# Optimization experiments

Hardware: AMD Instinct MI355X
Metric: run time of the kernel (lower is better)

## Reference

```python
import jax, jax.numpy as jnp
import numpy as np

BS = 8192
NUM_CLASSES = 400
D = 768


def _bilin_from_14(m14, Y, X, eH, eW):
    # Value of bilinear-resize(m14 -> (eH,eW)) at integer pixel (Y,X), computed on the fly.
    # torch F.interpolate(align_corners=False): src = (dst+0.5)*in/out - 0.5, clamped at 0.
    # m14: (bs,14,14); Y,X: (bs,14) float integer-valued coords; eH,eW: (bs,) float.
    sy = jnp.maximum((Y + 0.5) * 14.0 / eH[:, None] - 0.5, 0.0)
    sx = jnp.maximum((X + 0.5) * 14.0 / eW[:, None] - 0.5, 0.0)
    r0f = jnp.floor(sy); c0f = jnp.floor(sx)
    r0 = r0f.astype(jnp.int32); r1 = jnp.minimum(r0 + 1, 13)
    c0 = c0f.astype(jnp.int32); c1 = jnp.minimum(c0 + 1, 13)
    fy = sy - r0f; fx = sx - c0f
    b = jnp.arange(m14.shape[0])[:, None, None]
    g00 = m14[b, r0[:, :, None], c0[:, None, :]]
    g01 = m14[b, r0[:, :, None], c1[:, None, :]]
    g10 = m14[b, r1[:, :, None], c0[:, None, :]]
    g11 = m14[b, r1[:, :, None], c1[:, None, :]]
    wy = fy[:, :, None]; wx = fx[:, None, :]
    return g00 * (1 - wy) * (1 - wx) + g01 * (1 - wy) * wx + g10 * wy * (1 - wx) + g11 * wy * wx


def _get_mask(attn, o_pos, e_pos):
    # Fused, fully-batched equivalent of the per-sample python loop:
    #   resize 14x14 -> (eH,eW) bilinear; crop (top,left,oH,oW); resize -> 14x14 bilinear.
    # The final resize only reads the intermediate grid at 4 integer points per output
    # pixel, so we evaluate those points lazily via _bilin_from_14 (exact, no Emax grid).
    bs = attn.shape[0]
    m14 = attn.reshape(bs, 14, 14)
    eH = e_pos[:, 2].astype(jnp.float32); eW = e_pos[:, 3].astype(jnp.float32)
    top = (o_pos[:, 0] - e_pos[:, 0]).astype(jnp.float32)
    left = (o_pos[:, 1] - e_pos[:, 1]).astype(jnp.float32)
    oH = o_pos[:, 2].astype(jnp.float32); oW = o_pos[:, 3].astype(jnp.float32)
    i = jnp.arange(14, dtype=jnp.float32)[None, :]
    ty = jnp.maximum((i + 0.5) * oH[:, None] / 14.0 - 0.5, 0.0)  # (bs,14) coords in crop
    tx = jnp.maximum((i + 0.5) * oW[:, None] / 14.0 - 0.5, 0.0)
    y0 = jnp.floor(ty); y1 = jnp.minimum(y0 + 1.0, oH[:, None] - 1.0); wy = ty - y0
    x0 = jnp.floor(tx); x1 = jnp.minimum(x0 + 1.0, oW[:, None] - 1.0); wx = tx - x0
    Y0 = top[:, None] + y0; Y1 = top[:, None] + y1  # absolute rows in (eH,eW) grid
    X0 = left[:, None] + x0; X1 = left[:, None] + x1
    v00 = _bilin_from_14(m14, Y0, X0, eH, eW)
    v01 = _bilin_from_14(m14, Y0, X1, eH, eW)
    v10 = _bilin_from_14(m14, Y1, X0, eH, eW)
    v11 = _bilin_from_14(m14, Y1, X1, eH, eW)
    wyc = wy[:, :, None]; wxc = wx[:, None, :]
    out = v00 * (1 - wyc) * (1 - wxc) + v01 * (1 - wyc) * wxc + v10 * wyc * (1 - wxc) + v11 * wyc * wxc
    return out.reshape(bs, 196)


def _get_att_mask(attention, ratio=0.5):
    bs = attention.shape[0]
    a14 = attention.reshape(bs, 14, 14)
    # bilinear 14->7 with align_corners=False samples at frac 0.5 == 2x2 average pool
    a7 = a14.reshape(bs, 7, 2, 7, 2).mean(axis=(2, 4))
    flat = a7.reshape(bs, 49)
    n_keep = int(49 * ratio) + 1  # argsort desc, take top N+1 = 25
    _, idx = jax.lax.top_k(flat, n_keep)
    masks = jnp.ones((bs, 49), dtype=bool)
    masks = masks.at[jnp.arange(bs)[:, None], idx].set(False)
    m7 = masks.reshape(bs, 7, 7)
    full = jnp.repeat(jnp.repeat(m7, 2, axis=1), 2, axis=2)
    return full.reshape(bs, 196)


def setup_inputs() -> dict:
    key = jax.random.key(0)
    k1, k2, k3 = jax.random.split(key, 3)
    attn = jax.random.uniform(k1, (BS, 196), dtype=jnp.float32)
    rng = np.random.default_rng(0)
    IMG = 224
    eH = rng.integers(112, IMG + 1, BS); eW = rng.integers(112, IMG + 1, BS)
    eT = rng.integers(0, IMG - eH + 1); eL = rng.integers(0, IMG - eW + 1)
    def box():
        h = rng.integers(56, eH + 1); w = rng.integers(56, eW + 1)
        t = eT + rng.integers(0, eH - h + 1); l = eL + rng.integers(0, eW - w + 1)
        return np.stack([t, l, h, w], axis=1)
    e = np.stack([eT, eL, eH, eW], axis=1)
    pos = np.stack([box(), box(), e], axis=1).astype(np.int32)  # (BS,3,4)
    image_embed = jax.random.normal(k2, (2 * BS, D), dtype=jnp.float32)
    W = jax.random.normal(k3, (NUM_CLASSES, D), dtype=jnp.float32) * 0.02
    b = jnp.zeros((NUM_CLASSES,), dtype=jnp.float32)
    return {"attn": attn, "pos": jnp.asarray(pos), "image_embed": image_embed, "W": W, "b": b}


def reference(attn, pos, image_embed, W, b):
    cm1 = _get_mask(attn, pos[:, 0], pos[:, 2])
    mask1 = _get_att_mask(cm1)
    cm2 = _get_mask(attn, pos[:, 1], pos[:, 2])
    mask2 = _get_att_mask(cm2)
    mask = jnp.concatenate([mask1, mask2], axis=0)  # (2*bs,196) bool, fed to masked encoder
    logits = image_embed @ W.T + b
    return logits, mask
```

## Files before the change

### kernel.cpp

```cpp
#include <hip/hip_runtime.h>
#include <hip/hip_bf16.h>
#include <stdint.h>
#include <type_traits>

#define BSAMP 8192
#define NCLS 400
#define DIM 768
#define LOGITS_SIZE (16384LL * 400LL)
#define GEMM_BLOCKS 256
#define MASK_BLOCKS 4096
#define W_ELEMS (NCLS * DIM)

typedef __attribute__((ext_vector_type(8))) short short8;
typedef __attribute__((ext_vector_type(4))) float floatx4;

__device__ inline unsigned int packbf(float a, float b) {
    unsigned int ua = __float_as_uint(a) + 0x8000u;
    unsigned int ub = __float_as_uint(b) + 0x8000u;
    return __builtin_amdgcn_perm(ub, ua, 0x07060302u);
}

__device__ inline short8 cvt8(float4 lo, float4 hi) {
    union { unsigned int u[4]; short8 s; } r;
    r.u[0] = packbf(lo.x, lo.y);
    r.u[1] = packbf(lo.z, lo.w);
    r.u[2] = packbf(hi.x, hi.y);
    r.u[3] = packbf(hi.z, hi.w);
    return r.s;
}

__device__ inline void gload16(const void* g, void* l) {
    __builtin_amdgcn_global_load_lds((const __attribute__((address_space(1))) void*)g,
                                     (__attribute__((address_space(3))) void*)l, 16, 0, 0);
}

__global__ void cvtW_kernel(const float* __restrict__ W, unsigned short* __restrict__ ws) {
    int i = (blockIdx.x * 256 + threadIdx.x) * 4;
    if (i < W_ELEMS) {
        float4 f = *(const float4*)(W + i);
        uint2 r;
        r.x = packbf(f.x, f.y);
        r.y = packbf(f.z, f.w);
        *(uint2*)(ws + i) = r;
    }
}

__device__ inline float tap4(const float* m14, int r0, int c0, float fy, float fx) {
    int r1 = min(r0 + 1, 13);
    int c1 = min(c0 + 1, 13);
    float g00 = m14[r0 * 14 + c0];
    float g01 = m14[r0 * 14 + c1];
    float g10 = m14[r1 * 14 + c0];
    float g11 = m14[r1 * 14 + c1];
    return g00 * (1.f - fy) * (1.f - fx) + g01 * (1.f - fy) * fx +
           g10 * fy * (1.f - fx) + g11 * fy * fx;
}

struct GemmSm { unsigned short B[2][400 * 64]; };

template <bool USE_WS>
__global__ __launch_bounds__(512, 2) void gemm_kernel(const float* __restrict__ E,
                                                      const float* __restrict__ W,
                                                      const float* __restrict__ bias,
                                                      const unsigned short* __restrict__ wsW,
                                                      float* __restrict__ out) {
    __shared__ __align__(16) GemmSm sg;

    const int bx = blockIdx.x;
    const int t  = threadIdx.x;
    const int wv = t >> 6, ln = t & 63;

    const int m0 = bx * 64;
    const int quad = ln >> 4, l16 = ln & 15;

    const int half    = wv >> 2;
    const int NT      = half ? 12 : 13;
    const int colBase = half ? 208 : 0;

    const float* aptr = E + (size_t)(m0 + (wv & 3) * 16 + l16) * DIM + quad * 8;

    floatx4 acc[13];
#pragma unroll
    for (int ni = 0; ni < 13; ++ni) acc[ni] = (floatx4){0.f, 0.f, 0.f, 0.f};

    if constexpr (USE_WS) {
        auto stageB = [&](int s, int buf) {
            unsigned short* base = &sg.B[buf][0];
            for (int c = wv; c < 50; c += 8) {
                int row = c * 8 + (ln >> 3);
                const unsigned short* src = wsW + (size_t)row * DIM + s * 64 +
                                            ((ln >> 2) & 1) * 32 +
                                            8 * ((ln & 3) ^ ((row >> 1) & 3));
                gload16(src, base + c * 512);
            }
        };

        float4 pf[2][2];
        auto LDA = [&](int it, int d) {
            pf[d][0] = *(const float4*)(aptr + it * 32);
            pf[d][1] = *(const float4*)(aptr + it * 32 + 4);
        };

        stageB(0, 0);
        LDA(0, 0);
        LDA(1, 1);
        __syncthreads();

#pragma unroll
        for (int s = 0; s < 12; ++s) {
            if (s < 11) stageB(s + 1, (s + 1) & 1);
#pragma unroll
            for (int kk = 0; kk < 2; ++kk) {
                const int it = s * 2 + kk;
                const int pb = it & 1;
                short8 af = cvt8(pf[pb][0], pf[pb][1]);
                if (it < 22) LDA(it + 2, pb);
                __builtin_amdgcn_sched_barrier(0);
                const unsigned short* bb = &sg.B[s & 1][0];
#pragma unroll
                for (int ni = 0; ni < 13; ++ni) {
                    if (ni < NT) {
                        int row = colBase + ni * 16 + l16;
                        short8 bfr = *(const short8*)(bb + row * 64 + kk * 32 +
                                                      8 * (quad ^ ((row >> 1) & 3)));
                        acc[ni] = __builtin_amdgcn_mfma_f32_16x16x32_bf16(af, bfr, acc[ni], 0, 0, 0);
                    }
                }
            }
            __syncthreads();
        }
    } else {
        for (int it = 0; it < 24; ++it) {
            short8 af = cvt8(*(const float4*)(aptr + it * 32), *(const float4*)(aptr + it * 32 + 4));
#pragma unroll
            for (int ni = 0; ni < 13; ++ni) {
                if (ni < NT) {
                    const float* wp = W + (size_t)(colBase + ni * 16 + l16) * DIM + it * 32 + quad * 8;
                    short8 bfr = cvt8(*(const float4*)wp, *(const float4*)(wp + 4));
                    acc[ni] = __builtin_amdgcn_mfma_f32_16x16x32_bf16(af, bfr, acc[ni], 0, 0, 0);
                }
            }
        }
    }

    const int rowBase = m0 + (wv & 3) * 16 + quad * 4;
#pragma unroll
    for (int ni = 0; ni < 13; ++ni) {
        if (ni < NT) {
            int col = colBase + ni * 16 + l16;
            float bv = bias[col];
#pragma unroll
            for (int r = 0; r < 4; ++r) {
                out[(size_t)(rowBase + r) * NCLS + col] = acc[ni][r] + bv;
            }
        }
    }
}

struct MaskSm { float m14[4][208]; float a7[4][56]; float mv[4][56]; };

__global__ __launch_bounds__(256, 8) void mask_kernel(const float* __restrict__ attn,
                                                      const int* __restrict__ pos,
                                                      float* __restrict__ out) {
    __shared__ __align__(16) MaskSm sm;

    const int bx = blockIdx.x;
    const int t  = threadIdx.x;
    const int wv = t >> 6, ln = t & 63;

    const int p = bx * 4 + wv;
    const int b = p >> 1;
    const int o = p & 1;
    float* m14 = sm.m14[wv];

    for (int i = ln; i < 196; i += 64) m14[i] = attn[(size_t)b * 196 + i];

    const int* pb = pos + (size_t)b * 12;
    const float topf  = (float)(pb[o * 4 + 0] - pb[8]);
    const float leftf = (float)(pb[o * 4 + 1] - pb[9]);
    const float oH = (float)pb[o * 4 + 2];
    const float oW = (float)pb[o * 4 + 3];
    const float eH = (float)pb[10];
    const float eW = (float)pb[11];
    __syncthreads();

    const int i7 = ln / 7, j7 = ln - i7 * 7;
    if (ln < 49) {
        int   cI[2][2];  float cF[2][2];  float wxs[2];
        int   rI[2][2];  float rF[2][2];  float wys[2];
#pragma unroll
        for (int dx = 0; dx < 2; ++dx) {
            int ox = 2 * j7 + dx;
            float tx = fmaxf((ox + 0.5f) * oW / 14.0f - 0.5f, 0.0f);
            float x0 = floorf(tx);
            float x1 = fminf(x0 + 1.0f, oW - 1.0f);
            wxs[dx] = tx - x0;
            float X0 = leftf + x0, X1 = leftf + x1;
            float sx0 = fmaxf((X0 + 0.5f) * 14.0f / eW - 0.5f, 0.0f);
            float c0f = floorf(sx0);
            cI[dx][0] = (int)c0f; cF[dx][0] = sx0 - c0f;
            float sx1 = fmaxf((X1 + 0.5f) * 14.0f / eW - 0.5f, 0.0f);
            float c1f = floorf(sx1);
            cI[dx][1] = (int)c1f; cF[dx][1] = sx1 - c1f;
        }
#pragma unroll
        for (int dy = 0; dy < 2; ++dy) {
            int oy = 2 * i7 + dy;
            float ty = fmaxf((oy + 0.5f) * oH / 14.0f - 0.5f, 0.0f);
            float y0 = floorf(ty);
            float y1 = fminf(y0 + 1.0f, oH - 1.0f);
            wys[dy] = ty - y0;
            float Y0 = topf + y0, Y1 = topf + y1;
            float sy0 = fmaxf((Y0 + 0.5f) * 14.0f / eH - 0.5f, 0.0f);
            float r0f = floorf(sy0);
            rI[dy][0] = (int)r0f; rF[dy][0] = sy0 - r0f;
            float sy1 = fmaxf((Y1 + 0.5f) * 14.0f / eH - 0.5f, 0.0f);
            float r1f = floorf(sy1);
            rI[dy][1] = (int)r1f; rF[dy][1] = sy1 - r1f;
        }

        float s = 0.f;
#pragma unroll
        for (int dy = 0; dy < 2; ++dy) {
            float wy = wys[dy];
#pragma unroll
            for (int dx = 0; dx < 2; ++dx) {
                float wx = wxs[dx];
                float v00 = tap4(m14, rI[dy][0], cI[dx][0], rF[dy][0], cF[dx][0]);
                float v01 = tap4(m14, rI[dy][0], cI[dx][1], rF[dy][0], cF[dx][1]);
                float v10 = tap4(m14, rI[dy][1], cI[dx][0], rF[dy][1], cF[dx][0]);
                float v11 = tap4(m14, rI[dy][1], cI[dx][1], rF[dy][1], cF[dx][1]);
                float cm = v00 * (1.f - wy) * (1.f - wx) + v01 * (1.f - wy) * wx +
                           v10 * wy * (1.f - wx) + v11 * wy * wx;
                s += cm;
            }
        }
        sm.a7[wv][ln] = s * 0.25f;
    }
    __syncthreads();

    if (ln < 49) {
        float mine = sm.a7[wv][ln];
        int cnt = 0;
#pragma unroll 7
        for (int s2 = 0; s2 < 49; ++s2) {
            float v = sm.a7[wv][s2];
            cnt += (v > mine) || (v == mine && s2 < ln);
        }
        sm.mv[wv][ln] = (cnt < 25) ? 0.0f : 1.0f;
    }
    __syncthreads();

    float* ob = out + LOGITS_SIZE + (size_t)(o * BSAMP + b) * 196;
    for (int i = ln; i < 196; i += 64) {
        int oy = i / 14, ox = i - oy * 14;
        ob[i] = sm.mv[wv][(oy >> 1) * 7 + (ox >> 1)];
    }
}

extern "C" void kernel_launch(void* const* d_in, const int* in_sizes, int n_in,
                              void* d_out, int out_size, void* d_ws, size_t ws_size,
                              hipStream_t stream) {
    const float* attn = (const float*)d_in[0];
    const int*   pos  = (const int*)d_in[1];
    const float* E    = (const float*)d_in[2];
    const float* W    = (const float*)d_in[3];
    const float* bias = (const float*)d_in[4];
    float* out = (float*)d_out;

    if (ws_size >= (size_t)W_ELEMS * 2) {
        unsigned short* ws = (unsigned short*)d_ws;
        cvtW_kernel<<<300, 256, 0, stream>>>(W, ws);
        gemm_kernel<true><<<GEMM_BLOCKS, 512, 0, stream>>>(E, W, bias, ws, out);
    } else {
        gemm_kernel<false><<<GEMM_BLOCKS, 512, 0, stream>>>(E, W, bias, nullptr, out);
    }
    mask_kernel<<<MASK_BLOCKS, 256, 0, stream>>>(attn, pos, out);
}
```

Before: 148.3 us.

## Stage A tiles through LDS with async loads alongside B double-buffering

The fp32 activation tile is now loaded into a double-buffered LDS region with direct global-to-LDS 16-byte loads, using an XOR swizzle, in the same staging step as the bf16 weights. Previously each wave prefetched A straight from global into registers. Weight staging is rebalanced across waves with fixed unrolled counts, and __syncthreads is replaced by an explicit vmcnt wait plus s_barrier. The goal is coalesced, asynchronous A loads and fewer registers, but LDS use grows by 32KB per block, which may limit occupancy at 2 blocks per CU.

```diff
diff --git a/kernel.cpp b/kernel.cpp
--- a/kernel.cpp
+++ b/kernel.cpp
@@ -56,7 +56,10 @@
            g10 * fy * (1.f - fx) + g11 * fy * fx;
 }
 
-struct GemmSm { unsigned short B[2][400 * 64]; };
+struct GemmSm {
+    unsigned short B[2][400 * 64];
+    float          A[2][64 * 64];
+};
 
 template <bool USE_WS>
 __global__ __launch_bounds__(512, 2) void gemm_kernel(const float* __restrict__ E,
@@ -77,46 +80,65 @@
     const int NT      = half ? 12 : 13;
     const int colBase = half ? 208 : 0;
 
-    const float* aptr = E + (size_t)(m0 + (wv & 3) * 16 + l16) * DIM + quad * 8;
-
     floatx4 acc[13];
 #pragma unroll
     for (int ni = 0; ni < 13; ++ni) acc[ni] = (floatx4){0.f, 0.f, 0.f, 0.f};
 
     if constexpr (USE_WS) {
-        auto stageB = [&](int s, int buf) {
-            unsigned short* base = &sg.B[buf][0];
-            for (int c = wv; c < 50; c += 8) {
-                int row = c * 8 + (ln >> 3);
-                const unsigned short* src = wsW + (size_t)row * DIM + s * 64 +
-                                            ((ln >> 2) & 1) * 32 +
-                                            8 * ((ln & 3) ^ ((row >> 1) & 3));
-                gload16(src, base + c * 512);
+        auto stageAB = [&](int s, int buf) {
+            float* adst = &sg.A[buf][0];
+#pragma unroll
+            for (int i = 0; i < 2; ++i) {
+                int c = wv * 2 + i;
+                int r = c * 4 + (ln >> 4);
+                int u = ln & 15;
+                const float* src = E + (size_t)(m0 + r) * DIM + s * 64 + 4 * (u ^ (r & 15));
+                gload16(src, adst + c * 256 + ln * 4);
+            }
+            unsigned short* bdst = &sg.B[buf][0];
+            if (wv < 6) {
+#pragma unroll
+                for (int i = 0; i < 6; ++i) {
+                    int c = wv * 6 + i;
+                    int row = c * 8 + (ln >> 3);
+                    const unsigned short* src = wsW + (size_t)row * DIM + s * 64 +
+                                                ((ln >> 2) & 1) * 32 +
+                                                8 * ((ln & 3) ^ ((row >> 1) & 3));
+                    gload16(src, bdst + c * 512);
+                }
+            } else {
+#pragma unroll
+                for (int i = 0; i < 7; ++i) {
+                    int c = 36 + (wv - 6) * 7 + i;
+                    int row = c * 8 + (ln >> 3);
+                    const unsigned short* src = wsW + (size_t)row * DIM + s * 64 +
+                                                ((ln >> 2) & 1) * 32 +
+                                                8 * ((ln & 3) ^ ((row >> 1) & 3));
+                    gload16(src, bdst + c * 512);
+                }
             }
         };
 
-        float4 pf[2][2];
-        auto LDA = [&](int it, int d) {
-            pf[d][0] = *(const float4*)(aptr + it * 32);
-            pf[d][1] = *(const float4*)(aptr + it * 32 + 4);
-        };
-
-        stageB(0, 0);
-        LDA(0, 0);
-        LDA(1, 1);
-        __syncthreads();
+        stageAB(0, 0);
+        asm volatile("s_waitcnt vmcnt(0)" ::: "memory");
+        __builtin_amdgcn_s_barrier();
+        __builtin_amdgcn_sched_barrier(0);
+
+        const int arow = (wv & 3) * 16 + l16;
 
 #pragma unroll
         for (int s = 0; s < 12; ++s) {
-            if (s < 11) stageB(s + 1, (s + 1) & 1);
+            if (s < 11) stageAB(s + 1, (s + 1) & 1);
+            __builtin_amdgcn_sched_barrier(0);
+
+            const unsigned short* bb = &sg.B[s & 1][0];
+            const float*          ab = &sg.A[s & 1][0];
 #pragma unroll
             for (int kk = 0; kk < 2; ++kk) {
-                const int it = s * 2 + kk;
-                const int pb = it & 1;
-                short8 af = cvt8(pf[pb][0], pf[pb][1]);
-                if (it < 22) LDA(it + 2, pb);
-                __builtin_amdgcn_sched_barrier(0);
-                const unsigned short* bb = &sg.B[s & 1][0];
+                const int L0 = kk * 8 + quad * 2;
+                float4 lo = *(const float4*)(ab + arow * 64 + ((L0)     ^ l16) * 4);
+                float4 hi = *(const float4*)(ab + arow * 64 + ((L0 + 1) ^ l16) * 4);
+                short8 af = cvt8(lo, hi);
 #pragma unroll
                 for (int ni = 0; ni < 13; ++ni) {
                     if (ni < NT) {
@@ -127,9 +149,13 @@
                     }
                 }
             }
-            __syncthreads();
+
+            asm volatile("s_waitcnt vmcnt(0)" ::: "memory");
+            __builtin_amdgcn_s_barrier();
+            __builtin_amdgcn_sched_barrier(0);
         }
     } else {
+        const float* aptr = E + (size_t)(m0 + (wv & 3) * 16 + l16) * DIM + quad * 8;
         for (int it = 0; it < 24; ++it) {
             short8 af = cvt8(*(const float4*)(aptr + it * 32), *(const float4*)(aptr + it * 32 + 4));
 #pragma unroll
```

Result: no change. 146.5 us (-1.2%).

## Stage A tiles through LDS with 4-deep async pipeline and explicit vmcnt waits

Applied to the files above, without the earlier changes.

Replaces the double-buffered B staging with a 4-stage ring buffer of K=32 slices, and moves the activation (A) loads from direct register prefetch into LDS through the same async global-to-LDS path. Explicit s_waitcnt vmcnt counts and raw s_barrier replace __syncthreads, so three stages stay in flight. The aim is to hide global memory latency better and coalesce A loads. In exchange, LDS use per block grows, which could limit occupancy, and the hand-tuned wait counts are fragile.

```diff
diff --git a/kernel.cpp b/kernel.cpp
--- a/kernel.cpp
+++ b/kernel.cpp
@@ -56,7 +56,10 @@
            g10 * fy * (1.f - fx) + g11 * fy * fx;
 }
 
-struct GemmSm { unsigned short B[2][400 * 64]; };
+struct GemmSm {
+    unsigned short B[4][400 * 32];
+    float          A[4][8 * 256];
+};
 
 template <bool USE_WS>
 __global__ __launch_bounds__(512, 2) void gemm_kernel(const float* __restrict__ E,
@@ -77,59 +80,71 @@
     const int NT      = half ? 12 : 13;
     const int colBase = half ? 208 : 0;
 
-    const float* aptr = E + (size_t)(m0 + (wv & 3) * 16 + l16) * DIM + quad * 8;
-
     floatx4 acc[13];
 #pragma unroll
     for (int ni = 0; ni < 13; ++ni) acc[ni] = (floatx4){0.f, 0.f, 0.f, 0.f};
 
     if constexpr (USE_WS) {
-        auto stageB = [&](int s, int buf) {
-            unsigned short* base = &sg.B[buf][0];
-            for (int c = wv; c < 50; c += 8) {
-                int row = c * 8 + (ln >> 3);
-                const unsigned short* src = wsW + (size_t)row * DIM + s * 64 +
-                                            ((ln >> 2) & 1) * 32 +
-                                            8 * ((ln & 3) ^ ((row >> 1) & 3));
-                gload16(src, base + c * 512);
+        auto stage = [&](int s, int buf) {
+            gload16(E + (size_t)(m0 + ln) * DIM + s * 32 + wv * 4, &sg.A[buf][wv * 256]);
+            const int bu = 8 * ((ln & 3) ^ ((ln >> 3) & 3));
+            const int br = ln >> 2;
+#pragma unroll
+            for (int i = 0; i < 4; ++i) {
+                int c = wv + i * 8;
+                if (c < 25) {
+                    gload16(wsW + (size_t)(c * 16 + br) * DIM + s * 32 + bu,
+                            &sg.B[buf][c * 512]);
+                }
             }
         };
 
-        float4 pf[2][2];
-        auto LDA = [&](int it, int d) {
-            pf[d][0] = *(const float4*)(aptr + it * 32);
-            pf[d][1] = *(const float4*)(aptr + it * 32 + 4);
-        };
-
-        stageB(0, 0);
-        LDA(0, 0);
-        LDA(1, 1);
-        __syncthreads();
-
-#pragma unroll
-        for (int s = 0; s < 12; ++s) {
-            if (s < 11) stageB(s + 1, (s + 1) & 1);
-#pragma unroll
-            for (int kk = 0; kk < 2; ++kk) {
-                const int it = s * 2 + kk;
-                const int pb = it & 1;
-                short8 af = cvt8(pf[pb][0], pf[pb][1]);
-                if (it < 22) LDA(it + 2, pb);
+        const int arow4 = ((wv & 3) * 16 + l16) * 4;
+        const int bswz  = 8 * (quad ^ ((l16 >> 1) & 3));
+
+        stage(0, 0);
+        stage(1, 1);
+        stage(2, 2);
+        if (wv == 0) asm volatile("s_waitcnt vmcnt(10)" ::: "memory");
+        else         asm volatile("s_waitcnt vmcnt(8)"  ::: "memory");
+        __builtin_amdgcn_s_barrier();
+        __builtin_amdgcn_sched_barrier(0);
+
+#pragma unroll
+        for (int it = 0; it < 24; ++it) {
+            if (it <= 20) stage(it + 3, (it + 3) & 3);
+            __builtin_amdgcn_sched_barrier(0);
+
+            const float*          ab = &sg.A[it & 3][0];
+            const unsigned short* bb = &sg.B[it & 3][0];
+            float4 lo = *(const float4*)(ab + (quad * 2) * 256 + arow4);
+            float4 hi = *(const float4*)(ab + (quad * 2 + 1) * 256 + arow4);
+            short8 af = cvt8(lo, hi);
+#pragma unroll
+            for (int ni = 0; ni < 13; ++ni) {
+                if (ni < NT) {
+                    int row = colBase + ni * 16 + l16;
+                    short8 bfr = *(const short8*)(bb + row * 32 + bswz);
+                    acc[ni] = __builtin_amdgcn_mfma_f32_16x16x32_bf16(af, bfr, acc[ni], 0, 0, 0);
+                }
+            }
+
+            if (it < 23) {
+                if (it <= 20) {
+                    if (wv == 0) asm volatile("s_waitcnt vmcnt(10)" ::: "memory");
+                    else         asm volatile("s_waitcnt vmcnt(8)"  ::: "memory");
+                } else if (it == 21) {
+                    if (wv == 0) asm volatile("s_waitcnt vmcnt(5)" ::: "memory");
+                    else         asm volatile("s_waitcnt vmcnt(4)" ::: "memory");
+                } else {
+                    asm volatile("s_waitcnt vmcnt(0)" ::: "memory");
+                }
+                __builtin_amdgcn_s_barrier();
                 __builtin_amdgcn_sched_barrier(0);
-                const unsigned short* bb = &sg.B[s & 1][0];
-#pragma unroll
-                for (int ni = 0; ni < 13; ++ni) {
-                    if (ni < NT) {
-                        int row = colBase + ni * 16 + l16;
-                        short8 bfr = *(const short8*)(bb + row * 64 + kk * 32 +
-                                                      8 * (quad ^ ((row >> 1) & 3)));
-                        acc[ni] = __builtin_amdgcn_mfma_f32_16x16x32_bf16(af, bfr, acc[ni], 0, 0, 0);
-                    }
-                }
-            }
-            __syncthreads();
+            }
         }
     } else {
+        const float* aptr = E + (size_t)(m0 + (wv & 3) * 16 + l16) * DIM + quad * 8;
         for (int it = 0; it < 24; ++it) {
             short8 af = cvt8(*(const float4*)(aptr + it * 32), *(const float4*)(aptr + it * 32 + 4));
 #pragma unroll
```

Result: slower. 158.2 us (+6.7%).
